# Kernel tuning notes

Hardware: AMD Instinct MI355X
Metric: run time of the kernel (lower is better)

## Reference

```python
import jax, jax.numpy as jnp
import numpy as np

N = 50000      # nodes
E = 600000     # edges
F_IN = 128     # num_features
H = 128        # hidden_dim

def setup_inputs() -> dict:
    key = jax.random.key(0)
    k1, k2, k3 = jax.random.split(key, 3)
    x = jax.random.normal(k1, (N, F_IN), dtype=jnp.float32)
    W = jax.random.normal(k2, (F_IN, H), dtype=jnp.float32) * 0.05
    b = jnp.zeros((H,), dtype=jnp.float32)
    edge_index = jax.random.randint(k3, (2, E), 0, N, dtype=jnp.int64)
    return {"x": x, "W": W, "b": b, "edge_index": edge_index}

def reference(x, W, b, edge_index):
    # GCNConv (PyG default): add self-loops, symmetric deg^-1/2 normalization,
    # out[t] = sum_{(s,t) in E'} norm(s,t) * (x @ W)[s] + b, then relu.
    n = x.shape[0]
    loops = jnp.arange(n, dtype=edge_index.dtype)
    src = jnp.concatenate([edge_index[0], loops])  # [E+N]
    dst = jnp.concatenate([edge_index[1], loops])  # [E+N]
    xw = x @ W                                      # [N, H]
    deg = jax.ops.segment_sum(jnp.ones_like(dst, dtype=xw.dtype), dst,
                              num_segments=n)       # [N], >=1 due to self-loops
    dinv = jax.lax.rsqrt(deg)
    norm = dinv[src] * dinv[dst]                    # [E+N]
    msg = xw[src] * norm[:, None]                   # [E+N, H] gather
    agg = jax.ops.segment_sum(msg, dst, num_segments=n)  # [N, H] scatter-add
    out = jax.nn.relu(agg + b)
    # F.dropout(training=False) is identity in eval mode.
    return out
```

## Files before the change

### kernel.cpp

```cpp
#include <hip/hip_runtime.h>
#include <stdint.h>


#define FDIM 128
#define HDIM 128
#define SCAN_CHUNK 1024

using s8v   = __attribute__((ext_vector_type(8))) short;
using f32x4 = __attribute__((ext_vector_type(4))) float;

__device__ __forceinline__ unsigned bf16rn(float f) {
    unsigned u = __float_as_uint(f);
    return (u + 0x7fffu + ((u >> 16) & 1u)) >> 16;
}
__device__ __forceinline__ void upadd(unsigned w, float& lo, float& hi) {
    lo += __uint_as_float(w << 16);
    hi += __uint_as_float(w & 0xffff0000u);
}

__global__ __launch_bounds__(256) void k_setup(int* __restrict__ deg,
                                               const float* __restrict__ W,
                                               uint4* __restrict__ Warr, int n) {
    const int i = blockIdx.x * 256 + threadIdx.x;
    if (i < n) deg[i] = 0;
    if (i < (FDIM / 8) * HDIM) {
        const int chunk = i >> 7, nn = i & 127;
        float v[8];
#pragma unroll
        for (int j = 0; j < 8; ++j) v[j] = W[(chunk * 8 + j) * HDIM + nn];
        uint4 o;
        o.x = bf16rn(v[0]) | (bf16rn(v[1]) << 16);
        o.y = bf16rn(v[2]) | (bf16rn(v[3]) << 16);
        o.z = bf16rn(v[4]) | (bf16rn(v[5]) << 16);
        o.w = bf16rn(v[6]) | (bf16rn(v[7]) << 16);
        Warr[i] = o;
    }
}

__global__ __launch_bounds__(256) void k_count_slot(const int* __restrict__ dst,
                                                    int* __restrict__ deg,
                                                    int* __restrict__ slot, int e) {
    int i = blockIdx.x * 256 + threadIdx.x;
    if (i < e) slot[i] = atomicAdd(&deg[dst[i]], 1);
}

__global__ __launch_bounds__(256) void k_scan1(const int* __restrict__ deg,
                                               int* __restrict__ rowptr,
                                               int* __restrict__ partials,
                                               float* __restrict__ dinv, int n) {
    __shared__ int sdata[256];
    const int tid = threadIdx.x;
    const int base = blockIdx.x * SCAN_CHUNK + tid * 4;
    int v[4];
    int s = 0;
#pragma unroll
    for (int j = 0; j < 4; ++j) {
        int idx = base + j;
        v[j] = (idx < n) ? deg[idx] : 0;
        if (idx < n) dinv[idx] = rsqrtf((float)v[j] + 1.0f);
        s += v[j];
    }
    sdata[tid] = s;
    __syncthreads();
    for (int off = 1; off < 256; off <<= 1) {
        int t = (tid >= off) ? sdata[tid - off] : 0;
        __syncthreads();
        sdata[tid] += t;
        __syncthreads();
    }
    int run = sdata[tid] - s;
#pragma unroll
    for (int j = 0; j < 4; ++j) {
        int idx = base + j;
        if (idx < n) rowptr[idx] = run;
        run += v[j];
    }
    if (tid == 255) partials[blockIdx.x] = sdata[255];
}

__global__ __launch_bounds__(256) void k_scan23(int* __restrict__ rowptr,
                                                const int* __restrict__ partials,
                                                int n, int e) {
    const int i = blockIdx.x * 256 + threadIdx.x;
    const int nb = blockIdx.x >> 2;
    int s = 0;
    for (int k = 0; k < nb; ++k) s += partials[k];
    if (i < n) rowptr[i] += s;
    if (i == n) rowptr[n] = e;
}

__global__ __launch_bounds__(256) void k_fillpre(const int* __restrict__ src,
                                                 const int* __restrict__ dst,
                                                 const int* __restrict__ slot,
                                                 const int* __restrict__ rowptr,
                                                 int* __restrict__ elist,
                                                 const float* __restrict__ x,
                                                 const float* __restrict__ dinv,
                                                 uint4* __restrict__ xsb,
                                                 int e, int n, int fillBlocks) {
    if ((int)blockIdx.x < fillBlocks) {
        const int i = blockIdx.x * 256 + threadIdx.x;
        if (i < e) {
            const int d = dst[i];
            elist[rowptr[d] + slot[i]] = src[i];
        }
    } else {
        const long long idx = (long long)(blockIdx.x - fillBlocks) * 256 + threadIdx.x;
        if (idx >= (long long)n * (FDIM / 8)) return;
        const int node = (int)(idx >> 4);
        const float di = dinv[node];
        const float4* xp = (const float4*)x + idx * 2;
        const float4 a = xp[0], b = xp[1];
        uint4 o;
        o.x = bf16rn(a.x * di) | (bf16rn(a.y * di) << 16);
        o.y = bf16rn(a.z * di) | (bf16rn(a.w * di) << 16);
        o.z = bf16rn(b.x * di) | (bf16rn(b.y * di) << 16);
        o.w = bf16rn(b.z * di) | (bf16rn(b.w * di) << 16);
        xsb[idx] = o;
    }
}

__global__ __launch_bounds__(256) void k_gather_gemm(
    const uint4* __restrict__ xsb, const float* __restrict__ dinv,
    const int* __restrict__ rowptr, const int* __restrict__ elist,
    const uint4* __restrict__ Warr, const float* __restrict__ bias,
    float* __restrict__ out, int n) {
    __shared__ uint4 zlds[16][16];
    const int tid = threadIdx.x;
    const int r = tid >> 4, q = tid & 15;
    const int node = blockIdx.x * 16 + r;
    const int wave = tid >> 6, lane = tid & 63;
    const int l16 = lane & 15, lg = lane >> 4;

    s8v wf[2][4];
#pragma unroll
    for (int ntl = 0; ntl < 2; ++ntl)
#pragma unroll
        for (int ks = 0; ks < 4; ++ks)
            wf[ntl][ks] = *(const s8v*)&Warr[(ks * 4 + lg) * 128 +
                                             (wave * 2 + ntl) * 16 + l16];
    float bv0 = bias[(wave * 2 + 0) * 16 + l16];
    float bv1 = bias[(wave * 2 + 1) * 16 + l16];

    if (node < n) {
        const uint4* xq = xsb + q;
        float a0, a1, a2, a3, a4, a5, a6, a7;
        {
            const uint4 v = xq[(size_t)node * 16];
            a0 = __uint_as_float(v.x << 16); a1 = __uint_as_float(v.x & 0xffff0000u);
            a2 = __uint_as_float(v.y << 16); a3 = __uint_as_float(v.y & 0xffff0000u);
            a4 = __uint_as_float(v.z << 16); a5 = __uint_as_float(v.z & 0xffff0000u);
            a6 = __uint_as_float(v.w << 16); a7 = __uint_as_float(v.w & 0xffff0000u);
        }
        int j = rowptr[node];
        const int end = rowptr[node + 1];
        for (; j + 3 < end; j += 4) {
            const int s0 = elist[j], s1 = elist[j + 1];
            const int s2 = elist[j + 2], s3 = elist[j + 3];
            const uint4 u0 = xq[(size_t)s0 * 16];
            const uint4 u1 = xq[(size_t)s1 * 16];
            const uint4 u2 = xq[(size_t)s2 * 16];
            const uint4 u3 = xq[(size_t)s3 * 16];
            upadd(u0.x, a0, a1); upadd(u0.y, a2, a3); upadd(u0.z, a4, a5); upadd(u0.w, a6, a7);
            upadd(u1.x, a0, a1); upadd(u1.y, a2, a3); upadd(u1.z, a4, a5); upadd(u1.w, a6, a7);
            upadd(u2.x, a0, a1); upadd(u2.y, a2, a3); upadd(u2.z, a4, a5); upadd(u2.w, a6, a7);
            upadd(u3.x, a0, a1); upadd(u3.y, a2, a3); upadd(u3.z, a4, a5); upadd(u3.w, a6, a7);
        }
        for (; j < end; ++j) {
            const uint4 u = xq[(size_t)elist[j] * 16];
            upadd(u.x, a0, a1); upadd(u.y, a2, a3); upadd(u.z, a4, a5); upadd(u.w, a6, a7);
        }
        const float di = dinv[node];
        uint4 o;
        o.x = bf16rn(a0 * di) | (bf16rn(a1 * di) << 16);
        o.y = bf16rn(a2 * di) | (bf16rn(a3 * di) << 16);
        o.z = bf16rn(a4 * di) | (bf16rn(a5 * di) << 16);
        o.w = bf16rn(a6 * di) | (bf16rn(a7 * di) << 16);
        zlds[r][q ^ r] = o;
    }
    __syncthreads();

    s8v afr[4];
#pragma unroll
    for (int ks = 0; ks < 4; ++ks)
        afr[ks] = *(const s8v*)&zlds[l16][(ks * 4 + lg) ^ l16];

#pragma unroll
    for (int ntl = 0; ntl < 2; ++ntl) {
        f32x4 acc = (f32x4){0.f, 0.f, 0.f, 0.f};
#pragma unroll
        for (int ks = 0; ks < 4; ++ks)
            acc = __builtin_amdgcn_mfma_f32_16x16x32_bf16(afr[ks], wf[ntl][ks], acc, 0, 0, 0);
        const int col = (wave * 2 + ntl) * 16 + l16;
        const float bv = ntl ? bv1 : bv0;
#pragma unroll
        for (int rr = 0; rr < 4; ++rr) {
            const int row = blockIdx.x * 16 + lg * 4 + rr;
            if (row < n) out[(size_t)row * HDIM + col] = fmaxf(acc[rr] + bv, 0.0f);
        }
    }
}

__global__ __launch_bounds__(256) void k_fill_simple(const int* __restrict__ src,
                                                     const int* __restrict__ dst,
                                                     const int* __restrict__ slot,
                                                     const int* __restrict__ rowptr,
                                                     int* __restrict__ elist, int e) {
    int i = blockIdx.x * 256 + threadIdx.x;
    if (i < e) elist[rowptr[dst[i]] + slot[i]] = src[i];
}

__global__ __launch_bounds__(256) void k_gather_f32(const float* __restrict__ x,
                                                    const float* __restrict__ dinv,
                                                    const int* __restrict__ rowptr,
                                                    const int* __restrict__ elist,
                                                    float* __restrict__ z, int n) {
    const int lane = threadIdx.x & 31;
    const int node = blockIdx.x * 8 + (threadIdx.x >> 5);
    if (node >= n) return;
    const float di = dinv[node];
    float4 v = ((const float4*)(x + (size_t)node * FDIM))[lane];
    float4 sum;
    sum.x = di * v.x; sum.y = di * v.y; sum.z = di * v.z; sum.w = di * v.w;
    const int beg = rowptr[node], end = rowptr[node + 1];
    for (int j = beg; j < end; ++j) {
        const int s = elist[j];
        const float ds = dinv[s];
        const float4 u = ((const float4*)(x + (size_t)s * FDIM))[lane];
        sum.x = fmaf(ds, u.x, sum.x);
        sum.y = fmaf(ds, u.y, sum.y);
        sum.z = fmaf(ds, u.z, sum.z);
        sum.w = fmaf(ds, u.w, sum.w);
    }
    float4 o;
    o.x = di * sum.x; o.y = di * sum.y; o.z = di * sum.z; o.w = di * sum.w;
    ((float4*)(z + (size_t)node * FDIM))[lane] = o;
}

__global__ __launch_bounds__(512) void k_gemm_relu(const float* __restrict__ W,
                                                   const float* __restrict__ bias,
                                                   float* __restrict__ zo, int n) {
    __shared__ float Wl[FDIM * HDIM];
    __shared__ float xs[4][FDIM];
    const int t = threadIdx.x;
    const int h = t & (HDIM - 1);
    const int g = t >> 7;
    {
        const float4* W4 = (const float4*)W;
        float4* Wl4 = (float4*)Wl;
        for (int i = t; i < FDIM * HDIM / 4; i += 512) Wl4[i] = W4[i];
    }
    __syncthreads();
    const float bv = bias[h];
    const int nq = (n + 3) >> 2;
    for (int q = blockIdx.x; q < nq; q += gridDim.x) {
        const int row = q * 4 + g;
        if (row < n) xs[g][h] = zo[(size_t)row * HDIM + h];
        __syncthreads();
        if (row < n) {
            float acc = bv;
#pragma unroll
            for (int k = 0; k < FDIM; ++k)
                acc = fmaf(xs[g][k], Wl[k * HDIM + h], acc);
            zo[(size_t)row * HDIM + h] = fmaxf(acc, 0.0f);
        }
        __syncthreads();
    }
}

extern "C" void kernel_launch(void* const* d_in, const int* in_sizes, int n_in,
                              void* d_out, int out_size, void* d_ws, size_t ws_size,
                              hipStream_t stream) {
    const float* x = (const float*)d_in[0];
    const float* W = (const float*)d_in[1];
    const float* b = (const float*)d_in[2];
    const int* ei = (const int*)d_in[3];
    float* out = (float*)d_out;

    const int H = in_sizes[2];
    const int F = in_sizes[1] / H;
    const int N = in_sizes[0] / F;
    const int E = in_sizes[3] / 2;
    const int* srcp = ei;
    const int* dstp = ei + E;

    auto align256 = [](size_t v) { return (v + 255) & ~(size_t)255; };
    char* ws = (char*)d_ws;
    size_t off = 0;
    int* deg = (int*)(ws + off);      off += align256((size_t)N * 4);
    float* dinv = (float*)(ws + off); off += align256((size_t)N * 4);
    int* rowptr = (int*)(ws + off);   off += align256((size_t)(N + 1) * 4);
    int* slot = (int*)(ws + off);     off += align256((size_t)E * 4);
    int* partials = (int*)(ws + off); off += 256;
    int* elist = (int*)(ws + off);    off += align256((size_t)E * 4);
    const size_t base_off = off;
    uint4* xsb = (uint4*)(ws + off);  off += align256((size_t)N * FDIM * 2);
    uint4* Warr = (uint4*)(ws + off); off += align256((size_t)(FDIM / 8) * HDIM * 16);
    const bool fast = (ws_size >= off);

    const int nblk_scan1 = (N + SCAN_CHUNK - 1) / SCAN_CHUNK;

    if (fast) {
        k_setup<<<(N + 255) / 256, 256, 0, stream>>>(deg, W, Warr, N);
        k_count_slot<<<(E + 255) / 256, 256, 0, stream>>>(dstp, deg, slot, E);
        k_scan1<<<nblk_scan1, 256, 0, stream>>>(deg, rowptr, partials, dinv, N);
        k_scan23<<<(N + 1 + 255) / 256, 256, 0, stream>>>(rowptr, partials, N, E);
        const int fillBlocks = (E + 255) / 256;
        const long long nchunks = (long long)N * (FDIM / 8);
        const int preBlocks = (int)((nchunks + 255) / 256);
        k_fillpre<<<fillBlocks + preBlocks, 256, 0, stream>>>(
            srcp, dstp, slot, rowptr, elist, x, dinv, xsb, E, N, fillBlocks);
        k_gather_gemm<<<(N + 15) / 16, 256, 0, stream>>>(xsb, dinv, rowptr, elist,
                                                         Warr, b, out, N);
    } else {
        k_setup<<<(N + 255) / 256, 256, 0, stream>>>(deg, W, (uint4*)(ws + base_off), N);
        k_count_slot<<<(E + 255) / 256, 256, 0, stream>>>(dstp, deg, slot, E);
        k_scan1<<<nblk_scan1, 256, 0, stream>>>(deg, rowptr, partials, dinv, N);
        k_scan23<<<(N + 1 + 255) / 256, 256, 0, stream>>>(rowptr, partials, N, E);
        k_fill_simple<<<(E + 255) / 256, 256, 0, stream>>>(srcp, dstp, slot, rowptr, elist, E);
        k_gather_f32<<<(N + 7) / 8, 256, 0, stream>>>(x, dinv, rowptr, elist, out, N);
        k_gemm_relu<<<512, 512, 0, stream>>>(W, b, out, N);
    }
}
```

Before: 92.63 us.

## Restructure GCN preprocessing: single-pass scan, early x cast, per-edge dinv in gather

Replaces the two-kernel scan with a single-pass decoupled-lookback scan that chains block offsets through published flags, saving one launch. The bf16 cast of x now runs alongside the degree count and no longer pre-scales by dinv, so the fill kernel becomes edge-only. To compensate, the gather loads dinv of each neighbour and uses FMA, with a clamped unroll-by-4 loop in place of the remainder loop. Output stores become nontemporal. This costs extra dinv gathers per edge and relies on scan blocks being scheduled in order for the spin-wait.

```diff
diff --git a/kernel.cpp b/kernel.cpp
--- a/kernel.cpp
+++ b/kernel.cpp
@@ -13,17 +13,20 @@
     unsigned u = __float_as_uint(f);
     return (u + 0x7fffu + ((u >> 16) & 1u)) >> 16;
 }
-__device__ __forceinline__ void upadd(unsigned w, float& lo, float& hi) {
-    lo += __uint_as_float(w << 16);
-    hi += __uint_as_float(w & 0xffff0000u);
+__device__ __forceinline__ void upfma(unsigned w, float ds, float& lo, float& hi) {
+    lo = fmaf(ds, __uint_as_float(w << 16), lo);
+    hi = fmaf(ds, __uint_as_float(w & 0xffff0000u), hi);
 }
 
 __global__ __launch_bounds__(256) void k_setup(int* __restrict__ deg,
+                                               int* __restrict__ pub,
                                                const float* __restrict__ W,
-                                               uint4* __restrict__ Warr, int n) {
+                                               uint4* __restrict__ Warr,
+                                               int n, int nchunk, int packW) {
     const int i = blockIdx.x * 256 + threadIdx.x;
     if (i < n) deg[i] = 0;
-    if (i < (FDIM / 8) * HDIM) {
+    if (i < nchunk) pub[i] = 0;
+    if (packW && i < (FDIM / 8) * HDIM) {
         const int chunk = i >> 7, nn = i & 127;
         float v[8];
 #pragma unroll
@@ -37,20 +40,38 @@
     }
 }
 
-__global__ __launch_bounds__(256) void k_count_slot(const int* __restrict__ dst,
-                                                    int* __restrict__ deg,
-                                                    int* __restrict__ slot, int e) {
-    int i = blockIdx.x * 256 + threadIdx.x;
-    if (i < e) slot[i] = atomicAdd(&deg[dst[i]], 1);
-}
-
-__global__ __launch_bounds__(256) void k_scan1(const int* __restrict__ deg,
-                                               int* __restrict__ rowptr,
-                                               int* __restrict__ partials,
-                                               float* __restrict__ dinv, int n) {
+__global__ __launch_bounds__(256) void k_count_xcast(const int* __restrict__ dst,
+                                                     int* __restrict__ deg,
+                                                     int* __restrict__ slot,
+                                                     const float* __restrict__ x,
+                                                     uint4* __restrict__ xb,
+                                                     int e, int n, int fillBlocks) {
+    if ((int)blockIdx.x < fillBlocks) {
+        const int i = blockIdx.x * 256 + threadIdx.x;
+        if (i < e) slot[i] = atomicAdd(&deg[dst[i]], 1);
+    } else if (xb) {
+        const long long idx = (long long)(blockIdx.x - fillBlocks) * 256 + threadIdx.x;
+        if (idx >= (long long)n * (FDIM / 8)) return;
+        const float4* xp = (const float4*)x + idx * 2;
+        const float4 a = xp[0], b = xp[1];
+        uint4 o;
+        o.x = bf16rn(a.x) | (bf16rn(a.y) << 16);
+        o.y = bf16rn(a.z) | (bf16rn(a.w) << 16);
+        o.z = bf16rn(b.x) | (bf16rn(b.y) << 16);
+        o.w = bf16rn(b.z) | (bf16rn(b.w) << 16);
+        xb[idx] = o;
+    }
+}
+
+__global__ __launch_bounds__(256) void k_scan_dinv(const int* __restrict__ deg,
+                                                   int* __restrict__ rowptr,
+                                                   float* __restrict__ dinv,
+                                                   int* __restrict__ pub,
+                                                   int n, int e) {
     __shared__ int sdata[256];
-    const int tid = threadIdx.x;
-    const int base = blockIdx.x * SCAN_CHUNK + tid * 4;
+    __shared__ int sh_off;
+    const int tid = threadIdx.x, b = blockIdx.x;
+    const int base = b * SCAN_CHUNK + tid * 4;
     int v[4];
     int s = 0;
 #pragma unroll
@@ -68,60 +89,42 @@
         sdata[tid] += t;
         __syncthreads();
     }
-    int run = sdata[tid] - s;
+    if (tid == 255) {
+        int off = 0;
+        if (b > 0) {
+            int p;
+            do {
+                p = __hip_atomic_load(&pub[b - 1], __ATOMIC_ACQUIRE,
+                                      __HIP_MEMORY_SCOPE_AGENT);
+            } while (p == 0);
+            off = p - 1;
+        }
+        __hip_atomic_store(&pub[b], off + sdata[255] + 1, __ATOMIC_RELEASE,
+                           __HIP_MEMORY_SCOPE_AGENT);
+        sh_off = off;
+    }
+    __syncthreads();
+    int run = sdata[tid] - s + sh_off;
 #pragma unroll
     for (int j = 0; j < 4; ++j) {
         int idx = base + j;
         if (idx < n) rowptr[idx] = run;
         run += v[j];
     }
-    if (tid == 255) partials[blockIdx.x] = sdata[255];
-}
-
-__global__ __launch_bounds__(256) void k_scan23(int* __restrict__ rowptr,
-                                                const int* __restrict__ partials,
-                                                int n, int e) {
-    const int i = blockIdx.x * 256 + threadIdx.x;
-    const int nb = blockIdx.x >> 2;
-    int s = 0;
-    for (int k = 0; k < nb; ++k) s += partials[k];
-    if (i < n) rowptr[i] += s;
-    if (i == n) rowptr[n] = e;
-}
-
-__global__ __launch_bounds__(256) void k_fillpre(const int* __restrict__ src,
-                                                 const int* __restrict__ dst,
-                                                 const int* __restrict__ slot,
-                                                 const int* __restrict__ rowptr,
-                                                 int* __restrict__ elist,
-                                                 const float* __restrict__ x,
-                                                 const float* __restrict__ dinv,
-                                                 uint4* __restrict__ xsb,
-                                                 int e, int n, int fillBlocks) {
-    if ((int)blockIdx.x < fillBlocks) {
-        const int i = blockIdx.x * 256 + threadIdx.x;
-        if (i < e) {
-            const int d = dst[i];
-            elist[rowptr[d] + slot[i]] = src[i];
-        }
-    } else {
-        const long long idx = (long long)(blockIdx.x - fillBlocks) * 256 + threadIdx.x;
-        if (idx >= (long long)n * (FDIM / 8)) return;
-        const int node = (int)(idx >> 4);
-        const float di = dinv[node];
-        const float4* xp = (const float4*)x + idx * 2;
-        const float4 a = xp[0], b = xp[1];
-        uint4 o;
-        o.x = bf16rn(a.x * di) | (bf16rn(a.y * di) << 16);
-        o.y = bf16rn(a.z * di) | (bf16rn(a.w * di) << 16);
-        o.z = bf16rn(b.x * di) | (bf16rn(b.y * di) << 16);
-        o.w = bf16rn(b.z * di) | (bf16rn(b.w * di) << 16);
-        xsb[idx] = o;
-    }
+    if (b == (int)gridDim.x - 1 && tid == 255) rowptr[n] = e;
+}
+
+__global__ __launch_bounds__(256) void k_fill(const int* __restrict__ src,
+                                              const int* __restrict__ dst,
+                                              const int* __restrict__ slot,
+                                              const int* __restrict__ rowptr,
+                                              int* __restrict__ elist, int e) {
+    int i = blockIdx.x * 256 + threadIdx.x;
+    if (i < e) elist[rowptr[dst[i]] + slot[i]] = src[i];
 }
 
 __global__ __launch_bounds__(256) void k_gather_gemm(
-    const uint4* __restrict__ xsb, const float* __restrict__ dinv,
+    const uint4* __restrict__ xb, const float* __restrict__ dinv,
     const int* __restrict__ rowptr, const int* __restrict__ elist,
     const uint4* __restrict__ Warr, const float* __restrict__ bias,
     float* __restrict__ out, int n) {
@@ -132,6 +135,14 @@
     const int wave = tid >> 6, lane = tid & 63;
     const int l16 = lane & 15, lg = lane >> 4;
 
+    int beg = 0, end = 0;
+    float di = 0.0f;
+    if (node < n) {
+        beg = rowptr[node];
+        end = rowptr[node + 1];
+        di = dinv[node];
+    }
+
     s8v wf[2][4];
 #pragma unroll
     for (int ntl = 0; ntl < 2; ++ntl)
@@ -139,38 +150,41 @@
         for (int ks = 0; ks < 4; ++ks)
             wf[ntl][ks] = *(const s8v*)&Warr[(ks * 4 + lg) * 128 +
                                              (wave * 2 + ntl) * 16 + l16];
-    float bv0 = bias[(wave * 2 + 0) * 16 + l16];
-    float bv1 = bias[(wave * 2 + 1) * 16 + l16];
+    const float bv0 = bias[(wave * 2 + 0) * 16 + l16];
+    const float bv1 = bias[(wave * 2 + 1) * 16 + l16];
 
     if (node < n) {
-        const uint4* xq = xsb + q;
-        float a0, a1, a2, a3, a4, a5, a6, a7;
+        const uint4* xq = xb + q;
+        float a0 = 0.f, a1 = 0.f, a2 = 0.f, a3 = 0.f,
+              a4 = 0.f, a5 = 0.f, a6 = 0.f, a7 = 0.f;
         {
             const uint4 v = xq[(size_t)node * 16];
-            a0 = __uint_as_float(v.x << 16); a1 = __uint_as_float(v.x & 0xffff0000u);
-            a2 = __uint_as_float(v.y << 16); a3 = __uint_as_float(v.y & 0xffff0000u);
-            a4 = __uint_as_float(v.z << 16); a5 = __uint_as_float(v.z & 0xffff0000u);
-            a6 = __uint_as_float(v.w << 16); a7 = __uint_as_float(v.w & 0xffff0000u);
-        }
-        int j = rowptr[node];
-        const int end = rowptr[node + 1];
-        for (; j + 3 < end; j += 4) {
-            const int s0 = elist[j], s1 = elist[j + 1];
-            const int s2 = elist[j + 2], s3 = elist[j + 3];
+            upfma(v.x, di, a0, a1); upfma(v.y, di, a2, a3);
+            upfma(v.z, di, a4, a5); upfma(v.w, di, a6, a7);
+        }
+        for (int j = beg; j < end; j += 4) {
+            const int i1 = (j + 1 < end) ? j + 1 : end - 1;
+            const int i2 = (j + 2 < end) ? j + 2 : end - 1;
+            const int i3 = (j + 3 < end) ? j + 3 : end - 1;
+            const int s0 = elist[j], s1 = elist[i1];
+            const int s2 = elist[i2], s3 = elist[i3];
+            const float d0 = dinv[s0];
+            const float d1 = (j + 1 < end) ? dinv[s1] : 0.0f;
+            const float d2 = (j + 2 < end) ? dinv[s2] : 0.0f;
+            const float d3 = (j + 3 < end) ? dinv[s3] : 0.0f;
             const uint4 u0 = xq[(size_t)s0 * 16];
             const uint4 u1 = xq[(size_t)s1 * 16];
             const uint4 u2 = xq[(size_t)s2 * 16];
             const uint4 u3 = xq[(size_t)s3 * 16];
-            upadd(u0.x, a0, a1); upadd(u0.y, a2, a3); upadd(u0.z, a4, a5); upadd(u0.w, a6, a7);
-            upadd(u1.x, a0, a1); upadd(u1.y, a2, a3); upadd(u1.z, a4, a5); upadd(u1.w, a6, a7);
-            upadd(u2.x, a0, a1); upadd(u2.y, a2, a3); upadd(u2.z, a4, a5); upadd(u2.w, a6, a7);
-            upadd(u3.x, a0, a1); upadd(u3.y, a2, a3); upadd(u3.z, a4, a5); upadd(u3.w, a6, a7);
-        }
-        for (; j < end; ++j) {
-            const uint4 u = xq[(size_t)elist[j] * 16];
-            upadd(u.x, a0, a1); upadd(u.y, a2, a3); upadd(u.z, a4, a5); upadd(u.w, a6, a7);
-        }
-        const float di = dinv[node];
+            upfma(u0.x, d0, a0, a1); upfma(u0.y, d0, a2, a3);
+            upfma(u0.z, d0, a4, a5); upfma(u0.w, d0, a6, a7);
+            upfma(u1.x, d1, a0, a1); upfma(u1.y, d1, a2, a3);
+            upfma(u1.z, d1, a4, a5); upfma(u1.w, d1, a6, a7);
+            upfma(u2.x, d2, a0, a1); upfma(u2.y, d2, a2, a3);
+            upfma(u2.z, d2, a4, a5); upfma(u2.w, d2, a6, a7);
+            upfma(u3.x, d3, a0, a1); upfma(u3.y, d3, a2, a3);
+            upfma(u3.z, d3, a4, a5); upfma(u3.w, d3, a6, a7);
+        }
         uint4 o;
         o.x = bf16rn(a0 * di) | (bf16rn(a1 * di) << 16);
         o.y = bf16rn(a2 * di) | (bf16rn(a3 * di) << 16);
@@ -196,18 +210,11 @@
 #pragma unroll
         for (int rr = 0; rr < 4; ++rr) {
             const int row = blockIdx.x * 16 + lg * 4 + rr;
-            if (row < n) out[(size_t)row * HDIM + col] = fmaxf(acc[rr] + bv, 0.0f);
-        }
-    }
-}
-
-__global__ __launch_bounds__(256) void k_fill_simple(const int* __restrict__ src,
-                                                     const int* __restrict__ dst,
-                                                     const int* __restrict__ slot,
-                                                     const int* __restrict__ rowptr,
-                                                     int* __restrict__ elist, int e) {
-    int i = blockIdx.x * 256 + threadIdx.x;
-    if (i < e) elist[rowptr[dst[i]] + slot[i]] = src[i];
+            if (row < n)
+                __builtin_nontemporal_store(fmaxf(acc[rr] + bv, 0.0f),
+                                            &out[(size_t)row * HDIM + col]);
+        }
+    }
 }
 
 __global__ __launch_bounds__(256) void k_gather_f32(const float* __restrict__ x,
@@ -291,33 +298,32 @@
     float* dinv = (float*)(ws + off); off += align256((size_t)N * 4);
     int* rowptr = (int*)(ws + off);   off += align256((size_t)(N + 1) * 4);
     int* slot = (int*)(ws + off);     off += align256((size_t)E * 4);
-    int* partials = (int*)(ws + off); off += 256;
+    int* pub = (int*)(ws + off);      off += 1024;
     int* elist = (int*)(ws + off);    off += align256((size_t)E * 4);
-    const size_t base_off = off;
-    uint4* xsb = (uint4*)(ws + off);  off += align256((size_t)N * FDIM * 2);
+    uint4* xb = (uint4*)(ws + off);   off += align256((size_t)N * FDIM * 2);
     uint4* Warr = (uint4*)(ws + off); off += align256((size_t)(FDIM / 8) * HDIM * 16);
     const bool fast = (ws_size >= off);
 
-    const int nblk_scan1 = (N + SCAN_CHUNK - 1) / SCAN_CHUNK;
-
+    const int nblk_scan = (N + SCAN_CHUNK - 1) / SCAN_CHUNK;
+    const int fillBlocks = (E + 255) / 256;
+
+    k_setup<<<(N + 255) / 256, 256, 0, stream>>>(deg, pub, W, fast ? Warr : nullptr,
+                                                 N, nblk_scan, fast ? 1 : 0);
     if (fast) {
-        k_setup<<<(N + 255) / 256, 256, 0, stream>>>(deg, W, Warr, N);
-        k_count_slot<<<(E + 255) / 256, 256, 0, stream>>>(dstp, deg, slot, E);
-        k_scan1<<<nblk_scan1, 256, 0, stream>>>(deg, rowptr, partials, dinv, N);
-        k_scan23<<<(N + 1 + 255) / 256, 256, 0, stream>>>(rowptr, partials, N, E);
-        const int fillBlocks = (E + 255) / 256;
         const long long nchunks = (long long)N * (FDIM / 8);
-        const int preBlocks = (int)((nchunks + 255) / 256);
-        k_fillpre<<<fillBlocks + preBlocks, 256, 0, stream>>>(
-            srcp, dstp, slot, rowptr, elist, x, dinv, xsb, E, N, fillBlocks);
-        k_gather_gemm<<<(N + 15) / 16, 256, 0, stream>>>(xsb, dinv, rowptr, elist,
+        const int castBlocks = (int)((nchunks + 255) / 256);
+        k_count_xcast<<<fillBlocks + castBlocks, 256, 0, stream>>>(
+            dstp, deg, slot, x, xb, E, N, fillBlocks);
+    } else {
+        k_count_xcast<<<fillBlocks, 256, 0, stream>>>(dstp, deg, slot, x, nullptr,
+                                                      E, N, fillBlocks);
+    }
+    k_scan_dinv<<<nblk_scan, 256, 0, stream>>>(deg, rowptr, dinv, pub, N, E);
+    k_fill<<<fillBlocks, 256, 0, stream>>>(srcp, dstp, slot, rowptr, elist, E);
+    if (fast) {
+        k_gather_gemm<<<(N + 15) / 16, 256, 0, stream>>>(xb, dinv, rowptr, elist,
                                                          Warr, b, out, N);
     } else {
-        k_setup<<<(N + 255) / 256, 256, 0, stream>>>(deg, W, (uint4*)(ws + base_off), N);
-        k_count_slot<<<(E + 255) / 256, 256, 0, stream>>>(dstp, deg, slot, E);
-        k_scan1<<<nblk_scan1, 256, 0, stream>>>(deg, rowptr, partials, dinv, N);
-        k_scan23<<<(N + 1 + 255) / 256, 256, 0, stream>>>(rowptr, partials, N, E);
-        k_fill_simple<<<(E + 255) / 256, 256, 0, stream>>>(srcp, dstp, slot, rowptr, elist, E);
         k_gather_f32<<<(N + 7) / 8, 256, 0, stream>>>(x, dinv, rowptr, elist, out, N);
         k_gemm_relu<<<512, 512, 0, stream>>>(W, b, out, N);
     }
```

New measurement: 129.0 us. 1.39x slower.
